# Performance work log

Measured on AMD Instinct MI355X. Metric: run time of the kernel, lower is better.

## Reference

```python
import jax, jax.numpy as jnp
import numpy as np
import math

DIM = 1024
NUM_HEADS = 16
SHARED_HEADS = 1
ROUTED_HEADS = 3
HEAD_DIM = DIM // NUM_HEADS
B, N = 2, 2048


def setup_inputs() -> dict:
    key = jax.random.key(0)
    ks = jax.random.split(key, 16)
    s = 1.0 / math.sqrt(DIM)
    inp = {
        "x": jax.random.normal(ks[0], (B, N, DIM), dtype=jnp.float32),
        "Wq": jax.random.uniform(ks[1], (DIM, DIM), minval=-s, maxval=s),
        "bq": jax.random.uniform(ks[2], (DIM,), minval=-s, maxval=s),
        "Wk": jax.random.uniform(ks[3], (DIM, DIM), minval=-s, maxval=s),
        "bk": jax.random.uniform(ks[4], (DIM,), minval=-s, maxval=s),
        "Wv": jax.random.uniform(ks[5], (DIM, DIM), minval=-s, maxval=s),
        "bv": jax.random.uniform(ks[6], (DIM,), minval=-s, maxval=s),
        "Wp": jax.random.uniform(ks[7], (DIM, DIM), minval=-s, maxval=s),
        "bp": jax.random.uniform(ks[8], (DIM,), minval=-s, maxval=s),
        "Wr": jax.random.uniform(ks[9], (NUM_HEADS - SHARED_HEADS, DIM), minval=-s, maxval=s),
        "br": jax.random.uniform(ks[10], (NUM_HEADS - SHARED_HEADS,), minval=-s, maxval=s),
        "Ws": jax.random.uniform(ks[11], (2, DIM), minval=-s, maxval=s),
        "bs": jax.random.uniform(ks[12], (2,), minval=-s, maxval=s),
        # temperature init: log(exp(1/0.24)-1), shape (H,1,1)
        "temperature": jnp.full((NUM_HEADS, 1, 1), float(np.log(np.expm1(1.0 / 0.24))), dtype=jnp.float32),
        "query_embedding": 0.02 * jax.random.normal(ks[13], (NUM_HEADS, 1, HEAD_DIM), dtype=jnp.float32),
    }
    return inp


def reference(x, Wq, bq, Wk, bk, Wv, bv, Wp, bp, Wr, br, Ws, bs, temperature, query_embedding):
    Bsz, Nn, C = x.shape
    H, hd = NUM_HEADS, HEAD_DIM

    def heads(W, b):
        y = x @ W.T + b  # [B,N,C]
        return y.reshape(Bsz, Nn, H, hd).transpose(0, 2, 1, 3)  # [B,H,N,hd]

    q = heads(Wq, bq)
    k = heads(Wk, bk)
    v = heads(Wv, bv)

    q_norm = q / jnp.linalg.norm(q, axis=-1, keepdims=True)
    q_scaled = (q_norm + query_embedding[None]) * jax.nn.softplus(temperature)[None]
    attn = jnp.einsum("bhqd,bhkd->bhqk", q_scaled, k) / math.sqrt(hd)
    attn = jax.nn.softmax(attn, axis=-1)
    h = jnp.einsum("bhqk,bhkd->bhqd", attn, v)
    h = h.transpose(0, 2, 1, 3).reshape(Bsz, Nn, C)  # [B,N,C]

    # routed-head gating
    gates = jax.nn.softmax(h @ Wr.T + br, axis=-1)  # [B,N,H-shared]
    _, idx = jax.lax.top_k(gates, ROUTED_HEADS)
    # NOTE: original uses num_classes=num_heads-shared_heads for one_hot
    mask = jax.nn.one_hot(idx, H - SHARED_HEADS, dtype=gates.dtype).sum(axis=-2)
    routed_gates = gates * mask * ROUTED_HEADS

    sw = jax.nn.softmax(h @ Ws.T + bs, axis=-1)  # [B,N,2]
    shared_gates = sw * SHARED_HEADS
    weight_0 = sw * 2.0
    shared_gates = weight_0[..., 0:1] * shared_gates
    routed_gates = weight_0[..., 1:2] * routed_gates
    masked_gates = jnp.concatenate([shared_gates, routed_gates], axis=-1)

    # einsum('bnc,bnd->bnd') == per-token scalar sum over c times h
    out = h * masked_gates.sum(axis=-1, keepdims=True)
    return out @ Wp.T + bp
```

## Files before the change

kernel.cpp:

```cpp
#include <hip/hip_runtime.h>
#include <hip/hip_bf16.h>

typedef short s16x8 __attribute__((ext_vector_type(8)));
typedef float f32x4 __attribute__((ext_vector_type(4)));

__device__ __forceinline__ float b2f(unsigned short u) {
    union { unsigned int i; float f; } v;
    v.i = ((unsigned int)u) << 16;
    return v.f;
}
__device__ __forceinline__ unsigned short f2b(float f) {
    unsigned int x = __builtin_bit_cast(unsigned int, f);
    unsigned int r = (x + 0x7fffu + ((x >> 16) & 1u)) >> 16;
    return (unsigned short)r;
}
__device__ __forceinline__ unsigned int pkbf16(float a, float b) {
    union { __hip_bfloat162 h; unsigned int u; } v;
    v.h = __float22bfloat162_rn(make_float2(a, b));
    return v.u;
}
__device__ __forceinline__ float fast_exp2(float x) {
#if __has_builtin(__builtin_amdgcn_exp2f)
    return __builtin_amdgcn_exp2f(x);
#else
    return exp2f(x);
#endif
}

__device__ __forceinline__ void gl_lds16(const unsigned short* g, unsigned short* l) {
    __builtin_amdgcn_global_load_lds(
        (const __attribute__((address_space(1))) void*)g,
        (__attribute__((address_space(3))) void*)l, 16, 0, 0);
}


__device__ __forceinline__ void cvt8(const float* __restrict__ s,
                                     unsigned short* __restrict__ d, int i) {
    const float* p = s + (size_t)i * 8;
    float4 a = *(const float4*)p;
    float4 b = *(const float4*)(p + 4);
    unsigned int u0 = pkbf16(a.x, a.y), u1 = pkbf16(a.z, a.w);
    unsigned int u2 = pkbf16(b.x, b.y), u3 = pkbf16(b.z, b.w);
    uint4 o = {u0, u1, u2, u3};
    *(uint4*)&d[(size_t)i * 8] = o;
}

__global__ __launch_bounds__(256) void cvt_main(
    const float* __restrict__ x,  const float* __restrict__ Wq,
    const float* __restrict__ Wk, const float* __restrict__ Wv,
    const float* __restrict__ Wr, const float* __restrict__ Ws,
    const float* __restrict__ bq, const float* __restrict__ bk,
    const float* __restrict__ bv,
    unsigned short* __restrict__ xb, unsigned short* __restrict__ wqkv,
    unsigned short* __restrict__ wg, float* __restrict__ bqkv)
{
    int blk = blockIdx.x, t = threadIdx.x;
    if (blk < 2048)      cvt8(x,  xb,             blk * 256 + t);
    else if (blk < 2560) cvt8(Wq, wqkv,           (blk - 2048) * 256 + t);
    else if (blk < 3072) cvt8(Wk, wqkv + 1048576, (blk - 2560) * 256 + t);
    else if (blk < 3584) cvt8(Wv, wqkv + 2097152, (blk - 3072) * 256 + t);
    else if (blk < 3592) { int i = (blk - 3584) * 256 + t; if (i < 1920) cvt8(Wr, wg, i); }
    else if (blk < 3593) { int i = t; cvt8(Ws, wg + 15360, i); }
    else {
        int i = (blk - 3593) * 256 + t;
        bqkv[i] = (i < 1024) ? bq[i] : (i < 2048) ? bk[i - 1024] : bv[i - 2048];
    }
}

__global__ __launch_bounds__(256) void cvt_kernel(
    const float* __restrict__ src, unsigned short* __restrict__ dst, int n8)
{
    int i = blockIdx.x * 256 + threadIdx.x;
    if (i < n8) cvt8(src, dst, i);
}

__global__ __launch_bounds__(256) void qkv_gemm(
    const unsigned short* __restrict__ A,
    const unsigned short* __restrict__ Bw,
    const float* __restrict__ bias,
    unsigned short* __restrict__ Q, unsigned short* __restrict__ K,
    unsigned short* __restrict__ Vt)
{
    __shared__ __attribute__((aligned(16))) unsigned short As[128 * 64];
    __shared__ __attribute__((aligned(16))) unsigned short Bs[128 * 64];
    const int t = threadIdx.x;
    const int wave = t >> 6, lane = t & 63;
    const int m0 = blockIdx.x * 128, n0 = blockIdx.y * 128;
    const int wm = (wave >> 1) * 64, wn = (wave & 1) * 64;
    const int lr = lane & 15, lq = lane >> 4;
    const int srow = lane >> 3;
    const int scol = (((lane & 7) ^ srow) << 3);

    f32x4 acc[4][4];
#pragma unroll
    for (int i = 0; i < 4; ++i)
#pragma unroll
        for (int j = 0; j < 4; ++j) acc[i][j] = (f32x4){0.f, 0.f, 0.f, 0.f};

    for (int k0 = 0; k0 < 1024; k0 += 64) {
        __syncthreads();
#pragma unroll
        for (int i = 0; i < 4; ++i) {
            int rb = wave * 32 + i * 8;
            gl_lds16(&A[(size_t)(m0 + rb + srow) * 1024 + k0 + scol], &As[rb * 64]);
            gl_lds16(&Bw[(size_t)(n0 + rb + srow) * 1024 + k0 + scol], &Bs[rb * 64]);
        }
        __syncthreads();
#pragma unroll
        for (int kk = 0; kk < 64; kk += 32) {
            const int po = ((((kk >> 3) + lq) ^ (lr & 7)) << 3);
            s16x8 af[4], bf[4];
#pragma unroll
            for (int i = 0; i < 4; ++i)
                af[i] = *(const s16x8*)&As[(wm + i * 16 + lr) * 64 + po];
#pragma unroll
            for (int j = 0; j < 4; ++j)
                bf[j] = *(const s16x8*)&Bs[(wn + j * 16 + lr) * 64 + po];
#pragma unroll
            for (int i = 0; i < 4; ++i)
#pragma unroll
                for (int j = 0; j < 4; ++j)
                    acc[i][j] = __builtin_amdgcn_mfma_f32_16x16x32_bf16(af[i], bf[j], acc[i][j], 0, 0, 0);
        }
    }
    const int kind = n0 >> 10;
    const int nc = n0 & 1023;
    if (kind < 2) {
        unsigned short* Cm = kind ? K : Q;
#pragma unroll
        for (int j = 0; j < 4; ++j) {
            int cl = wn + j * 16 + lr;
            float bv = bias[n0 + cl];
#pragma unroll
            for (int i = 0; i < 4; ++i) {
                int rowb = m0 + wm + i * 16 + lq * 4;
                unsigned int u0 = pkbf16(acc[i][j][0] + bv, acc[i][j][1] + bv);
                unsigned int u1 = pkbf16(acc[i][j][2] + bv, acc[i][j][3] + bv);
                Cm[(size_t)(rowb + 0) * 1024 + nc + cl] = (unsigned short)u0;
                Cm[(size_t)(rowb + 1) * 1024 + nc + cl] = (unsigned short)(u0 >> 16);
                Cm[(size_t)(rowb + 2) * 1024 + nc + cl] = (unsigned short)u1;
                Cm[(size_t)(rowb + 3) * 1024 + nc + cl] = (unsigned short)(u1 >> 16);
            }
        }
    } else {
        const int bb = m0 >> 11;
#pragma unroll
        for (int j = 0; j < 4; ++j) {
            int col = nc + wn + j * 16 + lr;
            int hh = col >> 6, dd = col & 63;
            float bv = bias[n0 + wn + j * 16 + lr];
#pragma unroll
            for (int i = 0; i < 4; ++i) {
                int tokb = m0 + wm + i * 16 + lq * 4;
                int tloc = tokb & 2047;
                uint2 u;
                u.x = pkbf16(acc[i][j][0] + bv, acc[i][j][1] + bv);
                u.y = pkbf16(acc[i][j][2] + bv, acc[i][j][3] + bv);
                *(uint2*)&Vt[((size_t)(bb * 16 + hh) * 64 + dd) * 2048 + tloc] = u;
            }
        }
    }
}

__global__ __launch_bounds__(256) void attn_kernel(
    const unsigned short* __restrict__ Q,
    const unsigned short* __restrict__ Kb,
    const unsigned short* __restrict__ Vt,
    const float* __restrict__ temp,
    const float* __restrict__ qe,
    unsigned short* __restrict__ Hout)
{
    __shared__ __attribute__((aligned(16))) unsigned short Qs[128 * 64];
    __shared__ __attribute__((aligned(16))) unsigned short Ks[64 * 64];
    __shared__ __attribute__((aligned(16))) unsigned short Vs[64 * 64];
    __shared__ __attribute__((aligned(16))) unsigned short Ps[128 * 72];
    const int t = threadIdx.x, wave = t >> 6, lane = t & 63;
    const int lr = lane & 15, lq = lane >> 4;
    const int bh = blockIdx.y, b = bh >> 4, h = bh & 15;
    const int q0 = blockIdx.x * 128;
    const int srow = lane >> 3;
    const int scol = (((lane & 7) ^ srow) << 3);

#pragma unroll
    for (int i = 0; i < 4; ++i) {
        int rb = wave * 32 + i * 8;
        gl_lds16(&Q[(size_t)(b * 2048 + q0 + rb + srow) * 1024 + h * 64 + scol], &Qs[rb * 64]);
    }
    __syncthreads();

    {
        const int qr = t >> 1, part = t & 1;
        float tv = temp[h];
        float sp = ((tv > 20.f) ? tv : log1pf(__expf(tv))) * 0.18033688f;
        s16x8 frag[4];
        float v[4][8];
        float ss = 0.f;
#pragma unroll
        for (int c = 0; c < 4; ++c) {
            int pb = (((part * 4 + c) ^ (qr & 7)) << 3);
            frag[c] = *(const s16x8*)&Qs[qr * 64 + pb];
#pragma unroll
            for (int e = 0; e < 8; ++e) {
                v[c][e] = b2f((unsigned short)frag[c][e]);
                ss += v[c][e] * v[c][e];
            }
        }
        ss += __shfl_xor(ss, 1);
        float rn = rsqrtf(ss);
#pragma unroll
        for (int c = 0; c < 4; ++c) {
            const float* qh = qe + h * 64 + (part * 4 + c) * 8;
            s16x8 o;
#pragma unroll
            for (int e = 0; e < 8; e += 2) {
                unsigned int u = pkbf16((v[c][e] * rn + qh[e]) * sp,
                                        (v[c][e + 1] * rn + qh[e + 1]) * sp);
                o[e] = (short)u; o[e + 1] = (short)(u >> 16);
            }
            int pb = (((part * 4 + c) ^ (qr & 7)) << 3);
            *(s16x8*)&Qs[qr * 64 + pb] = o;
        }
    }

    f32x4 accO[2][4];
#pragma unroll
    for (int i = 0; i < 2; ++i)
#pragma unroll
        for (int j = 0; j < 4; ++j) accO[i][j] = (f32x4){0.f, 0.f, 0.f, 0.f};
    float lsum[2][4] = {{0.f, 0.f, 0.f, 0.f}, {0.f, 0.f, 0.f, 0.f}};

    for (int kc = 0; kc < 2048; kc += 64) {
        __syncthreads();
#pragma unroll
        for (int i = 0; i < 2; ++i) {
            int rb = wave * 16 + i * 8;
            gl_lds16(&Kb[(size_t)(b * 2048 + kc + rb + srow) * 1024 + h * 64 + scol], &Ks[rb * 64]);
            gl_lds16(&Vt[((size_t)(b * 16 + h) * 64 + rb + srow) * 2048 + kc + scol], &Vs[rb * 64]);
        }
        __syncthreads();

        f32x4 s[2][4];
#pragma unroll
        for (int i = 0; i < 2; ++i)
#pragma unroll
            for (int j = 0; j < 4; ++j) s[i][j] = (f32x4){0.f, 0.f, 0.f, 0.f};
#pragma unroll
        for (int kk = 0; kk < 64; kk += 32) {
            const int po = ((((kk >> 3) + lq) ^ (lr & 7)) << 3);
            s16x8 aq[2], bk[4];
#pragma unroll
            for (int i = 0; i < 2; ++i)
                aq[i] = *(const s16x8*)&Qs[(wave * 32 + i * 16 + lr) * 64 + po];
#pragma unroll
            for (int j = 0; j < 4; ++j)
                bk[j] = *(const s16x8*)&Ks[(j * 16 + lr) * 64 + po];
#pragma unroll
            for (int i = 0; i < 2; ++i)
#pragma unroll
                for (int j = 0; j < 4; ++j)
                    s[i][j] = __builtin_amdgcn_mfma_f32_16x16x32_bf16(aq[i], bk[j], s[i][j], 0, 0, 0);
        }

#pragma unroll
        for (int i = 0; i < 2; ++i)
#pragma unroll
            for (int r = 0; r < 4; ++r) {
                float p0 = fast_exp2(s[i][0][r]), p1 = fast_exp2(s[i][1][r]);
                float p2 = fast_exp2(s[i][2][r]), p3 = fast_exp2(s[i][3][r]);
                lsum[i][r] += (p0 + p1) + (p2 + p3);
                unsigned int ua = pkbf16(p0, p1), ub = pkbf16(p2, p3);
                int base = (wave * 32 + i * 16 + lq * 4 + r) * 72 + lr;
                Ps[base]      = (unsigned short)ua;
                Ps[base + 16] = (unsigned short)(ua >> 16);
                Ps[base + 32] = (unsigned short)ub;
                Ps[base + 48] = (unsigned short)(ub >> 16);
            }

#pragma unroll
        for (int kk = 0; kk < 64; kk += 32) {
            const int po = ((((kk >> 3) + lq) ^ (lr & 7)) << 3);
            s16x8 ap[2], bv[4];
#pragma unroll
            for (int i = 0; i < 2; ++i)
                ap[i] = *(const s16x8*)&Ps[(wave * 32 + i * 16 + lr) * 72 + kk + lq * 8];
#pragma unroll
            for (int j = 0; j < 4; ++j)
                bv[j] = *(const s16x8*)&Vs[(j * 16 + lr) * 64 + po];
#pragma unroll
            for (int i = 0; i < 2; ++i)
#pragma unroll
                for (int j = 0; j < 4; ++j)
                    accO[i][j] = __builtin_amdgcn_mfma_f32_16x16x32_bf16(ap[i], bv[j], accO[i][j], 0, 0, 0);
        }
    }

#pragma unroll
    for (int i = 0; i < 2; ++i)
#pragma unroll
        for (int r = 0; r < 4; ++r) {
            float l = lsum[i][r];
            l += __shfl_xor(l, 1); l += __shfl_xor(l, 2);
            l += __shfl_xor(l, 4); l += __shfl_xor(l, 8);
            float inv = 1.f / l;
            int row = q0 + wave * 32 + i * 16 + lq * 4 + r;
            size_t ob = (size_t)(b * 2048 + row) * 1024 + h * 64 + lr;
            unsigned int u0 = pkbf16(accO[i][0][r] * inv, accO[i][1][r] * inv);
            unsigned int u1 = pkbf16(accO[i][2][r] * inv, accO[i][3][r] * inv);
            Hout[ob]      = (unsigned short)u0;
            Hout[ob + 16] = (unsigned short)(u0 >> 16);
            Hout[ob + 32] = (unsigned short)u1;
            Hout[ob + 48] = (unsigned short)(u1 >> 16);
        }
}

__global__ __launch_bounds__(256) void gl_gemm(
    const unsigned short* __restrict__ Hb,
    const unsigned short* __restrict__ Wg,
    float* __restrict__ logits)
{
    __shared__ __attribute__((aligned(16))) unsigned short As[128 * 64];
    __shared__ __attribute__((aligned(16))) unsigned short Gs[32 * 64];
    const int t = threadIdx.x, wave = t >> 6, lane = t & 63;
    const int lr = lane & 15, lq = lane >> 4;
    const int m0 = blockIdx.x * 128;
    const int srow = lane >> 3;
    const int scol = (((lane & 7) ^ srow) << 3);

    f32x4 acc[2][2];
#pragma unroll
    for (int i = 0; i < 2; ++i)
#pragma unroll
        for (int j = 0; j < 2; ++j) acc[i][j] = (f32x4){0.f, 0.f, 0.f, 0.f};

    for (int k0 = 0; k0 < 1024; k0 += 64) {
        __syncthreads();
#pragma unroll
        for (int i = 0; i < 4; ++i) {
            int rb = wave * 32 + i * 8;
            gl_lds16(&Hb[(size_t)(m0 + rb + srow) * 1024 + k0 + scol], &As[rb * 64]);
        }
        {
            int row = wave * 8 + srow;
            int wr = (row > 16) ? 16 : row;
            gl_lds16(&Wg[(size_t)wr * 1024 + k0 + scol], &Gs[wave * 8 * 64]);
        }
        __syncthreads();
#pragma unroll
        for (int kk = 0; kk < 64; kk += 32) {
            const int po = ((((kk >> 3) + lq) ^ (lr & 7)) << 3);
            s16x8 af[2], gf[2];
#pragma unroll
            for (int i = 0; i < 2; ++i)
                af[i] = *(const s16x8*)&As[(wave * 32 + i * 16 + lr) * 64 + po];
#pragma unroll
            for (int j = 0; j < 2; ++j)
                gf[j] = *(const s16x8*)&Gs[(j * 16 + lr) * 64 + po];
#pragma unroll
            for (int i = 0; i < 2; ++i)
#pragma unroll
                for (int j = 0; j < 2; ++j)
                    acc[i][j] = __builtin_amdgcn_mfma_f32_16x16x32_bf16(af[i], gf[j], acc[i][j], 0, 0, 0);
        }
    }
#pragma unroll
    for (int i = 0; i < 2; ++i)
#pragma unroll
        for (int j = 0; j < 2; ++j) {
            int col = j * 16 + lr;
            int rowb = m0 + wave * 32 + i * 16 + lq * 4;
#pragma unroll
            for (int r = 0; r < 4; ++r)
                logits[(size_t)(rowb + r) * 32 + col] = acc[i][j][r];
        }
}

__global__ __launch_bounds__(256) void gate_apply(
    unsigned short* __restrict__ Hb,
    const float* __restrict__ logits,
    const float* __restrict__ br,
    const float* __restrict__ bs)
{
    const int tok = blockIdx.x, t = threadIdx.x;
    float lg[17];
#pragma unroll
    for (int j = 0; j < 17; ++j)
        lg[j] = logits[(size_t)tok * 32 + j] + ((j < 15) ? br[j] : bs[j - 15]);
    float mx = lg[0];
#pragma unroll
    for (int j = 1; j < 15; ++j) mx = fmaxf(mx, lg[j]);
    float sum = 0.f, v1 = -1.f, v2 = -1.f, v3 = -1.f;
#pragma unroll
    for (int j = 0; j < 15; ++j) {
        float e = __expf(lg[j] - mx);
        sum += e;
        if (e > v1)      { v3 = v2; v2 = v1; v1 = e; }
        else if (e > v2) { v3 = v2; v2 = e; }
        else if (e > v3) { v3 = e; }
    }
    float tops = (v1 + v2 + v3) / sum;
    float sm = fmaxf(lg[15], lg[16]);
    float e0 = __expf(lg[15] - sm), e1 = __expf(lg[16] - sm);
    float inv = 1.f / (e0 + e1);
    float g = 2.f * (e0 * inv) + 6.f * (e1 * inv) * tops;

    size_t base = (size_t)tok * 1024 + t * 4;
    ushort4 hr = *(const ushort4*)&Hb[base];
    unsigned int u0 = pkbf16(b2f(hr.x) * g, b2f(hr.y) * g);
    unsigned int u1 = pkbf16(b2f(hr.z) * g, b2f(hr.w) * g);
    uint2 o = {u0, u1};
    *(uint2*)&Hb[base] = o;
}

__global__ __launch_bounds__(256) void gemm64_out(
    const unsigned short* __restrict__ A,
    const unsigned short* __restrict__ Bw,
    const float* __restrict__ bias,
    float* __restrict__ C)
{
    __shared__ __attribute__((aligned(16))) unsigned short As[64 * 64];
    __shared__ __attribute__((aligned(16))) unsigned short Bs[128 * 64];
    const int t = threadIdx.x, wave = t >> 6, lane = t & 63;
    const int lr = lane & 15, lq = lane >> 4;
    const int m0 = blockIdx.x * 64, n0 = blockIdx.y * 128;
    const int wm = (wave >> 1) * 32, wn = (wave & 1) * 64;
    const int srow = lane >> 3;
    const int scol = (((lane & 7) ^ srow) << 3);

    f32x4 acc[2][4];
#pragma unroll
    for (int i = 0; i < 2; ++i)
#pragma unroll
        for (int j = 0; j < 4; ++j) acc[i][j] = (f32x4){0.f, 0.f, 0.f, 0.f};

    for (int k0 = 0; k0 < 1024; k0 += 64) {
        __syncthreads();
#pragma unroll
        for (int i = 0; i < 2; ++i) {
            int rb = wave * 16 + i * 8;
            gl_lds16(&A[(size_t)(m0 + rb + srow) * 1024 + k0 + scol], &As[rb * 64]);
        }
#pragma unroll
        for (int i = 0; i < 4; ++i) {
            int rb = wave * 32 + i * 8;
            gl_lds16(&Bw[(size_t)(n0 + rb + srow) * 1024 + k0 + scol], &Bs[rb * 64]);
        }
        __syncthreads();
#pragma unroll
        for (int kk = 0; kk < 64; kk += 32) {
            const int po = ((((kk >> 3) + lq) ^ (lr & 7)) << 3);
            s16x8 af[2], bf[4];
#pragma unroll
            for (int i = 0; i < 2; ++i)
                af[i] = *(const s16x8*)&As[(wm + i * 16 + lr) * 64 + po];
#pragma unroll
            for (int j = 0; j < 4; ++j)
                bf[j] = *(const s16x8*)&Bs[(wn + j * 16 + lr) * 64 + po];
#pragma unroll
            for (int i = 0; i < 2; ++i)
#pragma unroll
                for (int j = 0; j < 4; ++j)
                    acc[i][j] = __builtin_amdgcn_mfma_f32_16x16x32_bf16(af[i], bf[j], acc[i][j], 0, 0, 0);
        }
    }
#pragma unroll
    for (int j = 0; j < 4; ++j) {
        int col = n0 + wn + j * 16 + lr;
        float bv = bias[col];
#pragma unroll
        for (int i = 0; i < 2; ++i) {
            int rowb = m0 + wm + i * 16 + lq * 4;
#pragma unroll
            for (int r = 0; r < 4; ++r)
                C[(size_t)(rowb + r) * 1024 + col] = acc[i][j][r] + bv;
        }
    }
}

extern "C" void kernel_launch(void* const* d_in, const int* in_sizes, int n_in,
                              void* d_out, int out_size, void* d_ws, size_t ws_size,
                              hipStream_t stream)
{
    (void)in_sizes; (void)n_in; (void)out_size; (void)ws_size;
    const float* x   = (const float*)d_in[0];
    const float* Wq  = (const float*)d_in[1];
    const float* bq  = (const float*)d_in[2];
    const float* Wk  = (const float*)d_in[3];
    const float* bk  = (const float*)d_in[4];
    const float* Wv  = (const float*)d_in[5];
    const float* bv  = (const float*)d_in[6];
    const float* Wp  = (const float*)d_in[7];
    const float* bp  = (const float*)d_in[8];
    const float* Wr  = (const float*)d_in[9];
    const float* br  = (const float*)d_in[10];
    const float* Ws  = (const float*)d_in[11];
    const float* bs  = (const float*)d_in[12];
    const float* temperature = (const float*)d_in[13];
    const float* qe  = (const float*)d_in[14];
    float* out = (float*)d_out;

    const size_t MB = 1048576;
    unsigned short* qb     = (unsigned short*)d_ws;
    unsigned short* kb     = (unsigned short*)((char*)d_ws + 8 * MB);
    unsigned short* hb     = (unsigned short*)((char*)d_ws + 16 * MB);
    unsigned short* wqkv   = (unsigned short*)((char*)d_ws + 24 * MB);
    unsigned short* wpb    = wqkv;
    unsigned short* wg     = (unsigned short*)((char*)d_ws + 30 * MB);
    float*          bqkv   = (float*)((char*)d_ws + 30 * MB + 65536);
    float*          logits = (float*)((char*)d_ws + 30 * MB + 131072);
    unsigned short* xb = (unsigned short*)d_out;
    unsigned short* vt = xb + 4 * MB;

    dim3 blk(256);
    cvt_main<<<dim3(3605), blk, 0, stream>>>(x, Wq, Wk, Wv, Wr, Ws, bq, bk, bv,
                                             xb, wqkv, wg, bqkv);
    qkv_gemm<<<dim3(32, 24), blk, 0, stream>>>(xb, wqkv, bqkv, qb, kb, vt);
    cvt_kernel<<<dim3(512), blk, 0, stream>>>(Wp, wpb, 131072);
    attn_kernel<<<dim3(16, 32), blk, 0, stream>>>(qb, kb, vt, temperature, qe, hb);
    gl_gemm<<<dim3(32), blk, 0, stream>>>(hb, wg, logits);
    gate_apply<<<dim3(4096), blk, 0, stream>>>(hb, logits, br, bs);
    gemm64_out<<<dim3(64, 8), blk, 0, stream>>>(hb, wpb, bp, out);
}
```

Measured before the change: 240.1 us.

## Keep Q in registers, widen attention K tile, fuse gating into output GEMM

The attention kernel now keeps the normalized, scaled Q fragments in registers instead of LDS. That frees shared memory for 128-key K/V tiles, halving the number of barrier-separated load rounds, and V gets its own swizzle. The gate-logit GEMM and gate-apply kernels are merged into one split-K kernel (256 blocks instead of 32) that writes a per-token scalar gate. The scalar is applied in the output GEMM epilogue, so the read-modify-write pass over H disappears. Gating now multiplies the fp32 accumulator instead of the bf16-rounded H, which slightly changes rounding, and the extra register use from the Q fragments may cost occupancy.

```diff
diff --git a/kernel.cpp b/kernel.cpp
--- a/kernel.cpp
+++ b/kernel.cpp
@@ -8,11 +8,6 @@
     union { unsigned int i; float f; } v;
     v.i = ((unsigned int)u) << 16;
     return v.f;
-}
-__device__ __forceinline__ unsigned short f2b(float f) {
-    unsigned int x = __builtin_bit_cast(unsigned int, f);
-    unsigned int r = (x + 0x7fffu + ((x >> 16) & 1u)) >> 16;
-    return (unsigned short)r;
 }
 __device__ __forceinline__ unsigned int pkbf16(float a, float b) {
     union { __hip_bfloat162 h; unsigned int u; } v;
@@ -170,9 +165,8 @@
     const float* __restrict__ qe,
     unsigned short* __restrict__ Hout)
 {
-    __shared__ __attribute__((aligned(16))) unsigned short Qs[128 * 64];
-    __shared__ __attribute__((aligned(16))) unsigned short Ks[64 * 64];
-    __shared__ __attribute__((aligned(16))) unsigned short Vs[64 * 64];
+    __shared__ __attribute__((aligned(16))) unsigned short Ks[128 * 64];
+    __shared__ __attribute__((aligned(16))) unsigned short Vs[64 * 128];
     __shared__ __attribute__((aligned(16))) unsigned short Ps[128 * 72];
     const int t = threadIdx.x, wave = t >> 6, lane = t & 63;
     const int lr = lane & 15, lq = lane >> 4;
@@ -184,41 +178,38 @@
 #pragma unroll
     for (int i = 0; i < 4; ++i) {
         int rb = wave * 32 + i * 8;
-        gl_lds16(&Q[(size_t)(b * 2048 + q0 + rb + srow) * 1024 + h * 64 + scol], &Qs[rb * 64]);
+        gl_lds16(&Q[(size_t)(b * 2048 + q0 + rb + srow) * 1024 + h * 64 + scol], &Ks[rb * 64]);
     }
     __syncthreads();
 
-    {
-        const int qr = t >> 1, part = t & 1;
-        float tv = temp[h];
-        float sp = ((tv > 20.f) ? tv : log1pf(__expf(tv))) * 0.18033688f;
-        s16x8 frag[4];
-        float v[4][8];
+    float tv = temp[h];
+    float sp = ((tv > 20.f) ? tv : log1pf(__expf(tv))) * 0.18033688f;
+    s16x8 aq[2][2];
+#pragma unroll
+    for (int i = 0; i < 2; ++i) {
+        float v[2][8];
         float ss = 0.f;
 #pragma unroll
-        for (int c = 0; c < 4; ++c) {
-            int pb = (((part * 4 + c) ^ (qr & 7)) << 3);
-            frag[c] = *(const s16x8*)&Qs[qr * 64 + pb];
+        for (int kk = 0; kk < 2; ++kk) {
+            const int po = (((kk * 4 + lq) ^ (lr & 7)) << 3);
+            s16x8 f = *(const s16x8*)&Ks[(wave * 32 + i * 16 + lr) * 64 + po];
 #pragma unroll
             for (int e = 0; e < 8; ++e) {
-                v[c][e] = b2f((unsigned short)frag[c][e]);
-                ss += v[c][e] * v[c][e];
-            }
-        }
-        ss += __shfl_xor(ss, 1);
+                v[kk][e] = b2f((unsigned short)f[e]);
+                ss += v[kk][e] * v[kk][e];
+            }
+        }
+        ss += __shfl_xor(ss, 16); ss += __shfl_xor(ss, 32);
         float rn = rsqrtf(ss);
 #pragma unroll
-        for (int c = 0; c < 4; ++c) {
-            const float* qh = qe + h * 64 + (part * 4 + c) * 8;
-            s16x8 o;
+        for (int kk = 0; kk < 2; ++kk) {
+            const float* qh = qe + h * 64 + kk * 32 + lq * 8;
 #pragma unroll
             for (int e = 0; e < 8; e += 2) {
-                unsigned int u = pkbf16((v[c][e] * rn + qh[e]) * sp,
-                                        (v[c][e + 1] * rn + qh[e + 1]) * sp);
-                o[e] = (short)u; o[e + 1] = (short)(u >> 16);
-            }
-            int pb = (((part * 4 + c) ^ (qr & 7)) << 3);
-            *(s16x8*)&Qs[qr * 64 + pb] = o;
+                unsigned int u = pkbf16((v[kk][e] * rn + qh[e]) * sp,
+                                        (v[kk][e + 1] * rn + qh[e + 1]) * sp);
+                aq[i][kk][e] = (short)u; aq[i][kk][e + 1] = (short)(u >> 16);
+            }
         }
     }
 
@@ -229,68 +220,75 @@
         for (int j = 0; j < 4; ++j) accO[i][j] = (f32x4){0.f, 0.f, 0.f, 0.f};
     float lsum[2][4] = {{0.f, 0.f, 0.f, 0.f}, {0.f, 0.f, 0.f, 0.f}};
 
-    for (int kc = 0; kc < 2048; kc += 64) {
-        __syncthreads();
-#pragma unroll
-        for (int i = 0; i < 2; ++i) {
-            int rb = wave * 16 + i * 8;
+    for (int kc = 0; kc < 2048; kc += 128) {
+        __syncthreads();
+#pragma unroll
+        for (int i = 0; i < 4; ++i) {
+            int rb = wave * 32 + i * 8;
             gl_lds16(&Kb[(size_t)(b * 2048 + kc + rb + srow) * 1024 + h * 64 + scol], &Ks[rb * 64]);
-            gl_lds16(&Vt[((size_t)(b * 16 + h) * 64 + rb + srow) * 2048 + kc + scol], &Vs[rb * 64]);
-        }
-        __syncthreads();
-
-        f32x4 s[2][4];
-#pragma unroll
-        for (int i = 0; i < 2; ++i)
-#pragma unroll
-            for (int j = 0; j < 4; ++j) s[i][j] = (f32x4){0.f, 0.f, 0.f, 0.f};
-#pragma unroll
-        for (int kk = 0; kk < 64; kk += 32) {
-            const int po = ((((kk >> 3) + lq) ^ (lr & 7)) << 3);
-            s16x8 aq[2], bk[4];
+        }
+#pragma unroll
+        for (int i = 0; i < 4; ++i) {
+            int rb = wave * 16 + i * 4;
+            int vrow = rb + (lane >> 4);
+            int vcb = lane & 15;
+            gl_lds16(&Vt[((size_t)(b * 16 + h) * 64 + vrow) * 2048 + kc + ((vcb ^ (vrow & 7)) << 3)],
+                     &Vs[rb * 128]);
+        }
+        __syncthreads();
+
+#pragma unroll
+        for (int half = 0; half < 2; ++half) {
+            f32x4 s[2][4];
 #pragma unroll
             for (int i = 0; i < 2; ++i)
-                aq[i] = *(const s16x8*)&Qs[(wave * 32 + i * 16 + lr) * 64 + po];
-#pragma unroll
-            for (int j = 0; j < 4; ++j)
-                bk[j] = *(const s16x8*)&Ks[(j * 16 + lr) * 64 + po];
+#pragma unroll
+                for (int j = 0; j < 4; ++j) s[i][j] = (f32x4){0.f, 0.f, 0.f, 0.f};
+#pragma unroll
+            for (int kk = 0; kk < 2; ++kk) {
+                const int po = (((kk * 4 + lq) ^ (lr & 7)) << 3);
+                s16x8 bk[4];
+#pragma unroll
+                for (int j = 0; j < 4; ++j)
+                    bk[j] = *(const s16x8*)&Ks[(half * 64 + j * 16 + lr) * 64 + po];
+#pragma unroll
+                for (int i = 0; i < 2; ++i)
+#pragma unroll
+                    for (int j = 0; j < 4; ++j)
+                        s[i][j] = __builtin_amdgcn_mfma_f32_16x16x32_bf16(aq[i][kk], bk[j], s[i][j], 0, 0, 0);
+            }
+
 #pragma unroll
             for (int i = 0; i < 2; ++i)
 #pragma unroll
+                for (int r = 0; r < 4; ++r) {
+                    float p0 = fast_exp2(s[i][0][r]), p1 = fast_exp2(s[i][1][r]);
+                    float p2 = fast_exp2(s[i][2][r]), p3 = fast_exp2(s[i][3][r]);
+                    lsum[i][r] += (p0 + p1) + (p2 + p3);
+                    unsigned int ua = pkbf16(p0, p1), ub = pkbf16(p2, p3);
+                    int base = (wave * 32 + i * 16 + lq * 4 + r) * 72 + lr;
+                    Ps[base]      = (unsigned short)ua;
+                    Ps[base + 16] = (unsigned short)(ua >> 16);
+                    Ps[base + 32] = (unsigned short)ub;
+                    Ps[base + 48] = (unsigned short)(ub >> 16);
+                }
+
+#pragma unroll
+            for (int kk = 0; kk < 2; ++kk) {
+                const int vb = (((half * 8 + kk * 4 + lq) ^ (lr & 7)) << 3);
+                s16x8 ap[2], bv[4];
+#pragma unroll
+                for (int i = 0; i < 2; ++i)
+                    ap[i] = *(const s16x8*)&Ps[(wave * 32 + i * 16 + lr) * 72 + kk * 32 + lq * 8];
+#pragma unroll
                 for (int j = 0; j < 4; ++j)
-                    s[i][j] = __builtin_amdgcn_mfma_f32_16x16x32_bf16(aq[i], bk[j], s[i][j], 0, 0, 0);
-        }
-
-#pragma unroll
-        for (int i = 0; i < 2; ++i)
-#pragma unroll
-            for (int r = 0; r < 4; ++r) {
-                float p0 = fast_exp2(s[i][0][r]), p1 = fast_exp2(s[i][1][r]);
-                float p2 = fast_exp2(s[i][2][r]), p3 = fast_exp2(s[i][3][r]);
-                lsum[i][r] += (p0 + p1) + (p2 + p3);
-                unsigned int ua = pkbf16(p0, p1), ub = pkbf16(p2, p3);
-                int base = (wave * 32 + i * 16 + lq * 4 + r) * 72 + lr;
-                Ps[base]      = (unsigned short)ua;
-                Ps[base + 16] = (unsigned short)(ua >> 16);
-                Ps[base + 32] = (unsigned short)ub;
-                Ps[base + 48] = (unsigned short)(ub >> 16);
-            }
-
-#pragma unroll
-        for (int kk = 0; kk < 64; kk += 32) {
-            const int po = ((((kk >> 3) + lq) ^ (lr & 7)) << 3);
-            s16x8 ap[2], bv[4];
-#pragma unroll
-            for (int i = 0; i < 2; ++i)
-                ap[i] = *(const s16x8*)&Ps[(wave * 32 + i * 16 + lr) * 72 + kk + lq * 8];
-#pragma unroll
-            for (int j = 0; j < 4; ++j)
-                bv[j] = *(const s16x8*)&Vs[(j * 16 + lr) * 64 + po];
-#pragma unroll
-            for (int i = 0; i < 2; ++i)
-#pragma unroll
-                for (int j = 0; j < 4; ++j)
-                    accO[i][j] = __builtin_amdgcn_mfma_f32_16x16x32_bf16(ap[i], bv[j], accO[i][j], 0, 0, 0);
+                    bv[j] = *(const s16x8*)&Vs[(j * 16 + lr) * 128 + vb];
+#pragma unroll
+                for (int i = 0; i < 2; ++i)
+#pragma unroll
+                    for (int j = 0; j < 4; ++j)
+                        accO[i][j] = __builtin_amdgcn_mfma_f32_16x16x32_bf16(ap[i], bv[j], accO[i][j], 0, 0, 0);
+            }
         }
     }
 
@@ -313,108 +311,83 @@
         }
 }
 
-__global__ __launch_bounds__(256) void gl_gemm(
+__global__ __launch_bounds__(256) void gate_g(
     const unsigned short* __restrict__ Hb,
     const unsigned short* __restrict__ Wg,
-    float* __restrict__ logits)
-{
-    __shared__ __attribute__((aligned(16))) unsigned short As[128 * 64];
-    __shared__ __attribute__((aligned(16))) unsigned short Gs[32 * 64];
+    const float* __restrict__ br, const float* __restrict__ bs,
+    float* __restrict__ g)
+{
+    __shared__ __attribute__((aligned(16))) unsigned short As[4][16 * 64];
+    __shared__ __attribute__((aligned(16))) unsigned short Gs[4][32 * 64];
+    __shared__ float Lred[4][16][32];
     const int t = threadIdx.x, wave = t >> 6, lane = t & 63;
     const int lr = lane & 15, lq = lane >> 4;
-    const int m0 = blockIdx.x * 128;
+    const int m0 = blockIdx.x * 16;
     const int srow = lane >> 3;
     const int scol = (((lane & 7) ^ srow) << 3);
 
-    f32x4 acc[2][2];
-#pragma unroll
-    for (int i = 0; i < 2; ++i)
-#pragma unroll
-        for (int j = 0; j < 2; ++j) acc[i][j] = (f32x4){0.f, 0.f, 0.f, 0.f};
-
-    for (int k0 = 0; k0 < 1024; k0 += 64) {
-        __syncthreads();
+    f32x4 acc[2];
+    acc[0] = (f32x4){0.f, 0.f, 0.f, 0.f};
+    acc[1] = (f32x4){0.f, 0.f, 0.f, 0.f};
+
+    for (int k0 = wave * 64; k0 < 1024; k0 += 256) {
+        gl_lds16(&Hb[(size_t)(m0 + srow) * 1024 + k0 + scol], &As[wave][0]);
+        gl_lds16(&Hb[(size_t)(m0 + 8 + srow) * 1024 + k0 + scol], &As[wave][8 * 64]);
 #pragma unroll
         for (int i = 0; i < 4; ++i) {
-            int rb = wave * 32 + i * 8;
-            gl_lds16(&Hb[(size_t)(m0 + rb + srow) * 1024 + k0 + scol], &As[rb * 64]);
-        }
-        {
-            int row = wave * 8 + srow;
+            int row = i * 8 + srow;
             int wr = (row > 16) ? 16 : row;
-            gl_lds16(&Wg[(size_t)wr * 1024 + k0 + scol], &Gs[wave * 8 * 64]);
+            gl_lds16(&Wg[(size_t)wr * 1024 + k0 + scol], &Gs[wave][i * 8 * 64]);
         }
         __syncthreads();
 #pragma unroll
         for (int kk = 0; kk < 64; kk += 32) {
             const int po = ((((kk >> 3) + lq) ^ (lr & 7)) << 3);
-            s16x8 af[2], gf[2];
-#pragma unroll
-            for (int i = 0; i < 2; ++i)
-                af[i] = *(const s16x8*)&As[(wave * 32 + i * 16 + lr) * 64 + po];
-#pragma unroll
-            for (int j = 0; j < 2; ++j)
-                gf[j] = *(const s16x8*)&Gs[(j * 16 + lr) * 64 + po];
-#pragma unroll
-            for (int i = 0; i < 2; ++i)
-#pragma unroll
-                for (int j = 0; j < 2; ++j)
-                    acc[i][j] = __builtin_amdgcn_mfma_f32_16x16x32_bf16(af[i], gf[j], acc[i][j], 0, 0, 0);
-        }
-    }
-#pragma unroll
-    for (int i = 0; i < 2; ++i)
-#pragma unroll
-        for (int j = 0; j < 2; ++j) {
-            int col = j * 16 + lr;
-            int rowb = m0 + wave * 32 + i * 16 + lq * 4;
-#pragma unroll
-            for (int r = 0; r < 4; ++r)
-                logits[(size_t)(rowb + r) * 32 + col] = acc[i][j][r];
-        }
-}
-
-__global__ __launch_bounds__(256) void gate_apply(
-    unsigned short* __restrict__ Hb,
-    const float* __restrict__ logits,
-    const float* __restrict__ br,
-    const float* __restrict__ bs)
-{
-    const int tok = blockIdx.x, t = threadIdx.x;
-    float lg[17];
-#pragma unroll
-    for (int j = 0; j < 17; ++j)
-        lg[j] = logits[(size_t)tok * 32 + j] + ((j < 15) ? br[j] : bs[j - 15]);
-    float mx = lg[0];
-#pragma unroll
-    for (int j = 1; j < 15; ++j) mx = fmaxf(mx, lg[j]);
-    float sum = 0.f, v1 = -1.f, v2 = -1.f, v3 = -1.f;
-#pragma unroll
-    for (int j = 0; j < 15; ++j) {
-        float e = __expf(lg[j] - mx);
-        sum += e;
-        if (e > v1)      { v3 = v2; v2 = v1; v1 = e; }
-        else if (e > v2) { v3 = v2; v2 = e; }
-        else if (e > v3) { v3 = e; }
-    }
-    float tops = (v1 + v2 + v3) / sum;
-    float sm = fmaxf(lg[15], lg[16]);
-    float e0 = __expf(lg[15] - sm), e1 = __expf(lg[16] - sm);
-    float inv = 1.f / (e0 + e1);
-    float g = 2.f * (e0 * inv) + 6.f * (e1 * inv) * tops;
-
-    size_t base = (size_t)tok * 1024 + t * 4;
-    ushort4 hr = *(const ushort4*)&Hb[base];
-    unsigned int u0 = pkbf16(b2f(hr.x) * g, b2f(hr.y) * g);
-    unsigned int u1 = pkbf16(b2f(hr.z) * g, b2f(hr.w) * g);
-    uint2 o = {u0, u1};
-    *(uint2*)&Hb[base] = o;
+            s16x8 af = *(const s16x8*)&As[wave][lr * 64 + po];
+#pragma unroll
+            for (int j = 0; j < 2; ++j) {
+                s16x8 gf = *(const s16x8*)&Gs[wave][(j * 16 + lr) * 64 + po];
+                acc[j] = __builtin_amdgcn_mfma_f32_16x16x32_bf16(af, gf, acc[j], 0, 0, 0);
+            }
+        }
+    }
+#pragma unroll
+    for (int j = 0; j < 2; ++j)
+#pragma unroll
+        for (int r = 0; r < 4; ++r)
+            Lred[wave][lq * 4 + r][j * 16 + lr] = acc[j][r];
+    __syncthreads();
+    if (t < 16) {
+        float lg[17];
+#pragma unroll
+        for (int j = 0; j < 17; ++j)
+            lg[j] = Lred[0][t][j] + Lred[1][t][j] + Lred[2][t][j] + Lred[3][t][j]
+                  + ((j < 15) ? br[j] : bs[j - 15]);
+        float mx = lg[0];
+#pragma unroll
+        for (int j = 1; j < 15; ++j) mx = fmaxf(mx, lg[j]);
+        float sum = 0.f, v1 = -1.f, v2 = -1.f, v3 = -1.f;
+#pragma unroll
+        for (int j = 0; j < 15; ++j) {
+            float e = __expf(lg[j] - mx);
+            sum += e;
+            if (e > v1)      { v3 = v2; v2 = v1; v1 = e; }
+            else if (e > v2) { v3 = v2; v2 = e; }
+            else if (e > v3) { v3 = e; }
+        }
+        float tops = (v1 + v2 + v3) / sum;
+        float sm = fmaxf(lg[15], lg[16]);
+        float e0 = __expf(lg[15] - sm), e1 = __expf(lg[16] - sm);
+        float inv = 1.f / (e0 + e1);
+        g[m0 + t] = 2.f * (e0 * inv) + 6.f * (e1 * inv) * tops;
+    }
 }
 
 __global__ __launch_bounds__(256) void gemm64_out(
     const unsigned short* __restrict__ A,
     const unsigned short* __restrict__ Bw,
     const float* __restrict__ bias,
+    const float* __restrict__ g,
     float* __restrict__ C)
 {
     __shared__ __attribute__((aligned(16))) unsigned short As[64 * 64];
@@ -463,15 +436,17 @@
         }
     }
 #pragma unroll
-    for (int j = 0; j < 4; ++j) {
-        int col = n0 + wn + j * 16 + lr;
-        float bv = bias[col];
-#pragma unroll
-        for (int i = 0; i < 2; ++i) {
+    for (int i = 0; i < 2; ++i) {
+        const float4 gi = *(const float4*)&g[m0 + wm + i * 16 + lq * 4];
+        float gv[4] = {gi.x, gi.y, gi.z, gi.w};
+#pragma unroll
+        for (int j = 0; j < 4; ++j) {
+            int col = n0 + wn + j * 16 + lr;
+            float bv = bias[col];
             int rowb = m0 + wm + i * 16 + lq * 4;
 #pragma unroll
             for (int r = 0; r < 4; ++r)
-                C[(size_t)(rowb + r) * 1024 + col] = acc[i][j][r] + bv;
+                C[(size_t)(rowb + r) * 1024 + col] = acc[i][j][r] * gv[r] + bv;
         }
     }
 }
@@ -499,14 +474,14 @@
     float* out = (float*)d_out;
 
     const size_t MB = 1048576;
-    unsigned short* qb     = (unsigned short*)d_ws;
-    unsigned short* kb     = (unsigned short*)((char*)d_ws + 8 * MB);
-    unsigned short* hb     = (unsigned short*)((char*)d_ws + 16 * MB);
-    unsigned short* wqkv   = (unsigned short*)((char*)d_ws + 24 * MB);
-    unsigned short* wpb    = wqkv;
-    unsigned short* wg     = (unsigned short*)((char*)d_ws + 30 * MB);
-    float*          bqkv   = (float*)((char*)d_ws + 30 * MB + 65536);
-    float*          logits = (float*)((char*)d_ws + 30 * MB + 131072);
+    unsigned short* qb   = (unsigned short*)d_ws;
+    unsigned short* kb   = (unsigned short*)((char*)d_ws + 8 * MB);
+    unsigned short* hb   = (unsigned short*)((char*)d_ws + 16 * MB);
+    unsigned short* wqkv = (unsigned short*)((char*)d_ws + 24 * MB);
+    unsigned short* wpb  = wqkv;
+    unsigned short* wg   = (unsigned short*)((char*)d_ws + 30 * MB);
+    float*          bqkv = (float*)((char*)d_ws + 30 * MB + 65536);
+    float*          gbuf = (float*)((char*)d_ws + 30 * MB + 131072);
     unsigned short* xb = (unsigned short*)d_out;
     unsigned short* vt = xb + 4 * MB;
 
@@ -516,7 +491,6 @@
     qkv_gemm<<<dim3(32, 24), blk, 0, stream>>>(xb, wqkv, bqkv, qb, kb, vt);
     cvt_kernel<<<dim3(512), blk, 0, stream>>>(Wp, wpb, 131072);
     attn_kernel<<<dim3(16, 32), blk, 0, stream>>>(qb, kb, vt, temperature, qe, hb);
-    gl_gemm<<<dim3(32), blk, 0, stream>>>(hb, wg, logits);
-    gate_apply<<<dim3(4096), blk, 0, stream>>>(hb, logits, br, bs);
-    gemm64_out<<<dim3(64, 8), blk, 0, stream>>>(hb, wpb, bp, out);
-}
+    gate_g<<<dim3(256), blk, 0, stream>>>(hb, wg, br, bs, gbuf);
+    gemm64_out<<<dim3(64, 8), blk, 0, stream>>>(hb, wpb, bp, gbuf, out);
+}
```

New measurement: 223.0 us. -7.2%, faster.
